# Optimization experiments

Measured on AMD Instinct MI355X. Metric: run time of the kernel, lower is better.

The kernel has to match this reference:

```python
import jax, jax.numpy as jnp
import numpy as np


def _mha(x, pos, wq, bq, wk, bk, wv, bv, num_heads):
    # x: (B, S, Din); pos: (S, Din); w*: (Din, Dout); b*: (Dout,)
    x = x + pos  # learned positional embedding, broadcast over batch
    q = x @ wq + bq
    k = x @ wk + bk
    v = x @ wv + bv
    B, S, O = q.shape
    hd = O // num_heads
    q = q.reshape(B, S, num_heads, hd)
    k = k.reshape(B, S, num_heads, hd)
    v = v.reshape(B, S, num_heads, hd)
    scores = jnp.einsum('bshd,bthd->bhst', q, k) / jnp.sqrt(jnp.asarray(hd, x.dtype))
    attn = jax.nn.softmax(scores, axis=-1)
    out = jnp.einsum('bhst,bthd->bshd', attn, v)
    return out.reshape(B, S, O)


def setup_inputs() -> dict:
    key = jax.random.key(0)
    ks = jax.random.split(key, 16)
    B = 16384
    s = 0.3
    f32 = jnp.float32
    return {
        'state': jax.random.normal(ks[0], (B, 100), f32),
        # intraframe attention: Din=1, Dout=2, seq=10, heads=2
        'pos_intra': jax.random.normal(ks[1], (10, 1), f32) * s,
        'wq_intra': jax.random.normal(ks[2], (1, 2), f32) * s,
        'bq_intra': jnp.zeros((2,), f32),
        'wk_intra': jax.random.normal(ks[3], (1, 2), f32) * s,
        'bk_intra': jnp.zeros((2,), f32),
        'wv_intra': jax.random.normal(ks[4], (1, 2), f32) * s,
        'bv_intra': jnp.zeros((2,), f32),
        # interframe attention: Din=20, Dout=21, seq=10, heads=1
        'pos_inter': jax.random.normal(ks[5], (10, 20), f32) * s,
        'wq_inter': jax.random.normal(ks[6], (20, 21), f32) * s,
        'bq_inter': jnp.zeros((21,), f32),
        'wk_inter': jax.random.normal(ks[7], (20, 21), f32) * s,
        'bk_inter': jnp.zeros((21,), f32),
        'wv_inter': jax.random.normal(ks[8], (20, 21), f32) * s,
        'bv_inter': jnp.zeros((21,), f32),
    }


def reference(state, pos_intra, wq_intra, bq_intra, wk_intra, bk_intra,
              wv_intra, bv_intra, pos_inter, wq_inter, bq_inter, wk_inter,
              bk_inter, wv_inter, bv_inter):
    B = state.shape[0]
    # per-sample reshape (10,10,1) fused across the batch: (B*10 frames, 10 tokens, 1 feat)
    frames = state.reshape(B * 10, 10, 1)
    intra = _mha(frames, pos_intra, wq_intra, bq_intra, wk_intra, bk_intra,
                 wv_intra, bv_intra, num_heads=2)          # (B*10, 10, 2)
    x = intra.reshape(B, 10, 20)                            # (B, frames=10, 20)
    out = _mha(x, pos_inter, wq_inter, bq_inter, wk_inter, bk_inter,
               wv_inter, bv_inter, num_heads=1)             # (B, 10, 21)
    return out
```

## Files before the change

kernel.cpp:

```cpp
#include <hip/hip_runtime.h>

typedef __fp16 h2 __attribute__((ext_vector_type(2)));
typedef __fp16 h4 __attribute__((ext_vector_type(4)));
typedef __fp16 h8 __attribute__((ext_vector_type(8)));
typedef float  f4 __attribute__((ext_vector_type(4)));

#if __has_builtin(__builtin_amdgcn_fdot2)
#define FDOT2(a, b, c) __builtin_amdgcn_fdot2((a), (b), (c), false)
#else
#define FDOT2(a, b, c) ((c) + (float)(a)[0] * (float)(b)[0] + (float)(a)[1] * (float)(b)[1])
#endif

#define SPB 32
#define NT  320

struct SMa {
    __fp16 X [320 * 32];
    __fp16 WT[80 * 32];
    __fp16 pad_[640];
};
union UHead { SMa a; float sout[SPB * 210]; };

__global__ __launch_bounds__(NT, 2)
void crazy_attn_kernel(const float* __restrict__ state,
                       const float* __restrict__ pos_intra,
                       const float* __restrict__ wq_i, const float* __restrict__ bq_i,
                       const float* __restrict__ wk_i, const float* __restrict__ bk_i,
                       const float* __restrict__ wv_i, const float* __restrict__ bv_i,
                       const float* __restrict__ pos_inter,
                       const float* __restrict__ wq, const float* __restrict__ bq,
                       const float* __restrict__ wk, const float* __restrict__ bk,
                       const float* __restrict__ wv, const float* __restrict__ bv,
                       float* __restrict__ out, int B)
{
    __shared__ UHead uh;
    __shared__ __fp16 QKV[320 * 80];

    const int tid  = threadIdx.x;
    const int samp = tid / 10;
    const int r    = tid - samp * 10;
    const int gs   = blockIdx.x * SPB + samp;
    const int gsc  = (gs < B) ? gs : (B - 1);

    if (tid < 80) {
        const int c  = tid;
        const int g  = c / 24;
        const int cc = c - g * 24;
        const bool valid = (g < 3) && (cc < 21);
        const float* W  = (g == 1) ? wk : (g == 2) ? wv : wq;
        const float* Bb = (g == 1) ? bk : (g == 2) ? bv : bq;
        union { uint4 u4[4]; h2 hh[16]; } T;
        #pragma unroll
        for (int p = 0; p < 16; ++p) {
            const int j0 = 2 * p, j1 = 2 * p + 1;
            float lo = 0.f, hi = 0.f;
            if (valid) {
                lo = (j0 < 20) ? W[j0 * 21 + cc] : ((j0 == 20) ? Bb[cc] : 0.f);
                hi = (j1 < 20) ? W[j1 * 21 + cc] : ((j1 == 20) ? Bb[cc] : 0.f);
            }
            T.hh[p] = __builtin_amdgcn_cvt_pkrtz(lo, hi);
        }
        uint4* wd = (uint4*)&uh.a.WT[c * 32];
        wd[0] = T.u4[0]; wd[1] = T.u4[1]; wd[2] = T.u4[2]; wd[3] = T.u4[3];
    }

    {
        const float* sp = state + (size_t)gsc * 100 + r * 10;
        float xv[10];
        #pragma unroll
        for (int t = 0; t < 10; ++t) xv[t] = sp[t] + pos_intra[t];
        float xmx = xv[0], xmn = xv[0];
        #pragma unroll
        for (int t = 1; t < 10; ++t) { xmx = fmaxf(xmx, xv[t]); xmn = fminf(xmn, xv[t]); }

        float x[20];
        #pragma unroll
        for (int h = 0; h < 2; ++h) {
            const float wqh = wq_i[h], bqh = bq_i[h];
            const float wkh = wk_i[h];
            const float wvh = wv_i[h], bvh = bv_i[h];
            float vh[10], cs[10];
            #pragma unroll
            for (int t = 0; t < 10; ++t) {
                vh[t] = fmaf(xv[t], wvh, bvh);
                cs[t] = fmaf(xv[t], wqh, bqh) * wkh;
            }
            #pragma unroll
            for (int s = 0; s < 10; ++s) {
                const float c  = cs[s];
                const float mx = c * ((c >= 0.f) ? xmx : xmn);
                const float cL = c * 1.44269504f;
                const float mL = mx * 1.44269504f;
                float sum = 0.f, o = 0.f;
                #pragma unroll
                for (int t = 0; t < 10; ++t) {
                    const float e = __builtin_amdgcn_exp2f(fmaf(cL, xv[t], -mL));
                    sum += e; o = fmaf(e, vh[t], o);
                }
                x[s * 2 + h] = o * __builtin_amdgcn_rcpf(sum);
            }
        }
        const float* prow = pos_inter + r * 20;
        union { uint4 u4[4]; h2 hh[16]; } XR;
        #pragma unroll
        for (int p = 0; p < 10; ++p)
            XR.hh[p] = __builtin_amdgcn_cvt_pkrtz(x[2 * p] + prow[2 * p],
                                                  x[2 * p + 1] + prow[2 * p + 1]);
        XR.hh[10] = __builtin_amdgcn_cvt_pkrtz(1.0f, 0.f);
        const h2 z = __builtin_amdgcn_cvt_pkrtz(0.f, 0.f);
        XR.hh[11] = z; XR.hh[12] = z; XR.hh[13] = z; XR.hh[14] = z; XR.hh[15] = z;
        uint4* xd = (uint4*)&uh.a.X[(samp * 10 + r) * 32];
        xd[0] = XR.u4[0]; xd[1] = XR.u4[1]; xd[2] = XR.u4[2]; xd[3] = XR.u4[3];
    }
    __syncthreads();

    {
        const int l  = tid & 63;
        const int w  = tid >> 6;
        const int lr = l & 15, lh = l >> 4;
        h8 afrag[5];
        #pragma unroll
        for (int mt = 0; mt < 5; ++mt)
            afrag[mt] = *(const h8*)&uh.a.WT[(mt * 16 + lr) * 32 + lh * 8];
        #pragma unroll
        for (int i = 0; i < 4; ++i) {
            const int nt   = 4 * w + i;
            const int xrow = nt * 16 + lr;
            const h8 bfrag = *(const h8*)&uh.a.X[xrow * 32 + lh * 8];
            #pragma unroll
            for (int mt = 0; mt < 5; ++mt) {
                f4 acc = {0.f, 0.f, 0.f, 0.f};
                acc = __builtin_amdgcn_mfma_f32_16x16x32_f16(afrag[mt], bfrag, acc, 0, 0, 0);
                const int c0 = mt * 16 + lh * 4;
                union { h2 p2[2]; h4 p4; } P;
                P.p2[0] = __builtin_amdgcn_cvt_pkrtz(acc[0], acc[1]);
                P.p2[1] = __builtin_amdgcn_cvt_pkrtz(acc[2], acc[3]);
                *(h4*)&QKV[xrow * 80 + c0] = P.p4;
            }
        }
    }
    __syncthreads();

    {
        const __fp16* samprows = &QKV[samp * 10 * 80];
        union { uint4 u4[3]; h2 hh[12]; } Q;
        {
            const uint4* qsrc = (const uint4*)&samprows[r * 80];
            Q.u4[0] = qsrc[0]; Q.u4[1] = qsrc[1]; Q.u4[2] = qsrc[2];
        }
        float sc[10], m = -1e30f;
        #pragma unroll
        for (int t = 0; t < 10; ++t) {
            union { uint4 u4[3]; h2 hh[12]; } K;
            const uint4* ks = (const uint4*)&samprows[t * 80 + 24];
            K.u4[0] = ks[0]; K.u4[1] = ks[1]; K.u4[2] = ks[2];
            float d = 0.f;
            #pragma unroll
            for (int p = 0; p < 11; ++p) d = FDOT2(Q.hh[p], K.hh[p], d);
            d *= 0.21821789023599239f;
            sc[t] = d; m = fmaxf(m, d);
        }
        float sum = 0.f;
        #pragma unroll
        for (int t = 0; t < 10; ++t) {
            sc[t] = __builtin_amdgcn_exp2f((sc[t] - m) * 1.44269504f);
            sum += sc[t];
        }
        const float inv = __builtin_amdgcn_rcpf(sum);

        float acc[21];
        #pragma unroll
        for (int c = 0; c < 21; ++c) acc[c] = 0.f;
        #pragma unroll
        for (int t = 0; t < 10; ++t) {
            union { uint4 u4[3]; h2 hh[12]; } V;
            const uint4* vs = (const uint4*)&samprows[t * 80 + 48];
            V.u4[0] = vs[0]; V.u4[1] = vs[1]; V.u4[2] = vs[2];
            const float a = sc[t] * inv;
            #pragma unroll
            for (int c = 0; c < 21; ++c)
                acc[c] = fmaf(a, (float)V.hh[c >> 1][c & 1], acc[c]);
        }
        float* dst = &uh.sout[(samp * 10 + r) * 21];
        #pragma unroll
        for (int c = 0; c < 21; ++c) dst[c] = acc[c];
    }
    __syncthreads();

    {
        const int samp0 = blockIdx.x * SPB;
        const int nrem  = B - samp0;
        const int nval  = ((nrem < SPB) ? nrem : SPB) * 210;
        float* gdst = out + (size_t)samp0 * 210;
        if (nval == SPB * 210) {
            #pragma unroll
            for (int i = tid; i < SPB * 210 / 4; i += NT)
                ((f4*)gdst)[i] = ((const f4*)uh.sout)[i];
        } else {
            for (int i = tid; i < nval; i += NT) gdst[i] = uh.sout[i];
        }
    }
}

extern "C" void kernel_launch(void* const* d_in, const int* in_sizes, int n_in,
                              void* d_out, int out_size, void* d_ws, size_t ws_size,
                              hipStream_t stream) {
    const float* state     = (const float*)d_in[0];
    const float* pos_intra = (const float*)d_in[1];
    const float* wq_i      = (const float*)d_in[2];
    const float* bq_i      = (const float*)d_in[3];
    const float* wk_i      = (const float*)d_in[4];
    const float* bk_i      = (const float*)d_in[5];
    const float* wv_i      = (const float*)d_in[6];
    const float* bv_i      = (const float*)d_in[7];
    const float* pos_inter = (const float*)d_in[8];
    const float* wq        = (const float*)d_in[9];
    const float* bq        = (const float*)d_in[10];
    const float* wk        = (const float*)d_in[11];
    const float* bk        = (const float*)d_in[12];
    const float* wv        = (const float*)d_in[13];
    const float* bv        = (const float*)d_in[14];
    float* outp = (float*)d_out;

    const int B = in_sizes[0] / 100;
    const int grid = (B + SPB - 1) / SPB;
    hipLaunchKernelGGL(crazy_attn_kernel, dim3(grid), dim3(NT), 0, stream,
                       state, pos_intra, wq_i, bq_i, wk_i, bk_i, wv_i, bv_i,
                       pos_inter, wq, bq, wk, bk, wv, bv, outp, B);
}
```

Measured before the change: 27.06 us.

## Split each attention row across lane pairs with DPP reductions, doubling block threads

Doubles threads per block from 320 to 640. Each row's work in the intraframe and interframe attention is now split between two adjacent lanes: each lane handles half of the query positions or keys. Partial max, sum and output accumulators are combined with a DPP xor-1 lane swap. The MFMA stage gives each wave 2 tiles instead of 4. The intent is more parallelism and latency hiding per sample, at the cost of duplicated loads of xv/Q, extra cross-lane ops and a higher launch-bounds occupancy target that may constrain registers.

After: 25.97 us. 1.04x faster.

```diff
diff --git a/kernel.cpp b/kernel.cpp
--- a/kernel.cpp
+++ b/kernel.cpp
@@ -12,7 +12,12 @@
 #endif
 
 #define SPB 32
-#define NT  320
+#define NT  640
+
+__device__ __forceinline__ float dpp_xor1(float x) {
+    int i = __builtin_amdgcn_mov_dpp(__float_as_int(x), 0xB1, 0xF, 0xF, true);
+    return __int_as_float(i);
+}
 
 struct SMa {
     __fp16 X [320 * 32];
@@ -21,7 +26,7 @@
 };
 union UHead { SMa a; float sout[SPB * 210]; };
 
-__global__ __launch_bounds__(NT, 2)
+__global__ __launch_bounds__(NT, 5)
 void crazy_attn_kernel(const float* __restrict__ state,
                        const float* __restrict__ pos_intra,
                        const float* __restrict__ wq_i, const float* __restrict__ bq_i,
@@ -37,8 +42,9 @@
     __shared__ __fp16 QKV[320 * 80];
 
     const int tid  = threadIdx.x;
-    const int samp = tid / 10;
-    const int r    = tid - samp * 10;
+    const int e    = tid & 1;
+    const int rr   = (tid >> 1) % 10;
+    const int samp = tid / 20;
     const int gs   = blockIdx.x * SPB + samp;
     const int gsc  = (gs < B) ? gs : (B - 1);
 
@@ -65,7 +71,7 @@
     }
 
     {
-        const float* sp = state + (size_t)gsc * 100 + r * 10;
+        const float* sp = state + (size_t)gsc * 100 + rr * 10;
         float xv[10];
         #pragma unroll
         for (int t = 0; t < 10; ++t) xv[t] = sp[t] + pos_intra[t];
@@ -73,44 +79,47 @@
         #pragma unroll
         for (int t = 1; t < 10; ++t) { xmx = fmaxf(xmx, xv[t]); xmn = fminf(xmn, xv[t]); }
 
-        float x[20];
+        float res[2][5];
         #pragma unroll
         for (int h = 0; h < 2; ++h) {
             const float wqh = wq_i[h], bqh = bq_i[h];
             const float wkh = wk_i[h];
             const float wvh = wv_i[h], bvh = bv_i[h];
-            float vh[10], cs[10];
-            #pragma unroll
-            for (int t = 0; t < 10; ++t) {
-                vh[t] = fmaf(xv[t], wvh, bvh);
-                cs[t] = fmaf(xv[t], wqh, bqh) * wkh;
-            }
-            #pragma unroll
-            for (int s = 0; s < 10; ++s) {
-                const float c  = cs[s];
+            float vh[10];
+            #pragma unroll
+            for (int t = 0; t < 10; ++t) vh[t] = fmaf(xv[t], wvh, bvh);
+            #pragma unroll
+            for (int si = 0; si < 5; ++si) {
+                const float c0 = fmaf(xv[2 * si],     wqh, bqh) * wkh;
+                const float c1 = fmaf(xv[2 * si + 1], wqh, bqh) * wkh;
+                const float c  = e ? c1 : c0;
                 const float mx = c * ((c >= 0.f) ? xmx : xmn);
                 const float cL = c * 1.44269504f;
                 const float mL = mx * 1.44269504f;
                 float sum = 0.f, o = 0.f;
                 #pragma unroll
                 for (int t = 0; t < 10; ++t) {
-                    const float e = __builtin_amdgcn_exp2f(fmaf(cL, xv[t], -mL));
-                    sum += e; o = fmaf(e, vh[t], o);
+                    const float ex = __builtin_amdgcn_exp2f(fmaf(cL, xv[t], -mL));
+                    sum += ex; o = fmaf(ex, vh[t], o);
                 }
-                x[s * 2 + h] = o * __builtin_amdgcn_rcpf(sum);
+                res[h][si] = o * __builtin_amdgcn_rcpf(sum);
             }
         }
-        const float* prow = pos_inter + r * 20;
-        union { uint4 u4[4]; h2 hh[16]; } XR;
-        #pragma unroll
-        for (int p = 0; p < 10; ++p)
-            XR.hh[p] = __builtin_amdgcn_cvt_pkrtz(x[2 * p] + prow[2 * p],
-                                                  x[2 * p + 1] + prow[2 * p + 1]);
-        XR.hh[10] = __builtin_amdgcn_cvt_pkrtz(1.0f, 0.f);
-        const h2 z = __builtin_amdgcn_cvt_pkrtz(0.f, 0.f);
-        XR.hh[11] = z; XR.hh[12] = z; XR.hh[13] = z; XR.hh[14] = z; XR.hh[15] = z;
-        uint4* xd = (uint4*)&uh.a.X[(samp * 10 + r) * 32];
-        xd[0] = XR.u4[0]; xd[1] = XR.u4[1]; xd[2] = XR.u4[2]; xd[3] = XR.u4[3];
+        __fp16* xrow = &uh.a.X[(samp * 10 + rr) * 32];
+        const float* prow = pos_inter + rr * 20;
+        #pragma unroll
+        for (int si = 0; si < 5; ++si) {
+            const int s = 2 * si + e;
+            *(h2*)&xrow[2 * s] = __builtin_amdgcn_cvt_pkrtz(res[0][si] + prow[2 * s],
+                                                            res[1][si] + prow[2 * s + 1]);
+        }
+        const h2 z  = __builtin_amdgcn_cvt_pkrtz(0.f, 0.f);
+        const h2 bz = __builtin_amdgcn_cvt_pkrtz(1.0f, 0.f);
+        #pragma unroll
+        for (int j = 0; j < 3; ++j) {
+            const int k = 20 + 2 * (3 * e + j);
+            *(h2*)&xrow[k] = (e == 0 && j == 0) ? bz : z;
+        }
     }
     __syncthreads();
 
@@ -123,8 +132,8 @@
         for (int mt = 0; mt < 5; ++mt)
             afrag[mt] = *(const h8*)&uh.a.WT[(mt * 16 + lr) * 32 + lh * 8];
         #pragma unroll
-        for (int i = 0; i < 4; ++i) {
-            const int nt   = 4 * w + i;
+        for (int i = 0; i < 2; ++i) {
+            const int nt   = 2 * w + i;
             const int xrow = nt * 16 + lr;
             const h8 bfrag = *(const h8*)&uh.a.X[xrow * 32 + lh * 8];
             #pragma unroll
@@ -145,45 +154,55 @@
         const __fp16* samprows = &QKV[samp * 10 * 80];
         union { uint4 u4[3]; h2 hh[12]; } Q;
         {
-            const uint4* qsrc = (const uint4*)&samprows[r * 80];
+            const uint4* qsrc = (const uint4*)&samprows[rr * 80];
             Q.u4[0] = qsrc[0]; Q.u4[1] = qsrc[1]; Q.u4[2] = qsrc[2];
         }
-        float sc[10], m = -1e30f;
-        #pragma unroll
-        for (int t = 0; t < 10; ++t) {
+        float mysc[5];
+        #pragma unroll
+        for (int i = 0; i < 5; ++i) {
+            const int t = 2 * i + e;
             union { uint4 u4[3]; h2 hh[12]; } K;
             const uint4* ks = (const uint4*)&samprows[t * 80 + 24];
             K.u4[0] = ks[0]; K.u4[1] = ks[1]; K.u4[2] = ks[2];
             float d = 0.f;
             #pragma unroll
             for (int p = 0; p < 11; ++p) d = FDOT2(Q.hh[p], K.hh[p], d);
-            d *= 0.21821789023599239f;
-            sc[t] = d; m = fmaxf(m, d);
-        }
-        float sum = 0.f;
-        #pragma unroll
-        for (int t = 0; t < 10; ++t) {
-            sc[t] = __builtin_amdgcn_exp2f((sc[t] - m) * 1.44269504f);
-            sum += sc[t];
-        }
+            mysc[i] = d * 0.21821789023599239f;
+        }
+        float mymax = mysc[0];
+        #pragma unroll
+        for (int i = 1; i < 5; ++i) mymax = fmaxf(mymax, mysc[i]);
+        const float m = fmaxf(mymax, dpp_xor1(mymax));
+        float pe[5], psum = 0.f;
+        #pragma unroll
+        for (int i = 0; i < 5; ++i) {
+            pe[i] = __builtin_amdgcn_exp2f((mysc[i] - m) * 1.44269504f);
+            psum += pe[i];
+        }
+        const float sum = psum + dpp_xor1(psum);
         const float inv = __builtin_amdgcn_rcpf(sum);
 
         float acc[21];
         #pragma unroll
         for (int c = 0; c < 21; ++c) acc[c] = 0.f;
         #pragma unroll
-        for (int t = 0; t < 10; ++t) {
+        for (int i = 0; i < 5; ++i) {
+            const int t = 2 * i + e;
             union { uint4 u4[3]; h2 hh[12]; } V;
             const uint4* vs = (const uint4*)&samprows[t * 80 + 48];
             V.u4[0] = vs[0]; V.u4[1] = vs[1]; V.u4[2] = vs[2];
-            const float a = sc[t] * inv;
+            const float a = pe[i] * inv;
             #pragma unroll
             for (int c = 0; c < 21; ++c)
                 acc[c] = fmaf(a, (float)V.hh[c >> 1][c & 1], acc[c]);
         }
-        float* dst = &uh.sout[(samp * 10 + r) * 21];
-        #pragma unroll
-        for (int c = 0; c < 21; ++c) dst[c] = acc[c];
+        #pragma unroll
+        for (int c = 0; c < 21; ++c) acc[c] += dpp_xor1(acc[c]);
+        if (e == 0) {
+            float* dst = &uh.sout[(samp * 10 + rr) * 21];
+            #pragma unroll
+            for (int c = 0; c < 21; ++c) dst[c] = acc[c];
+        }
     }
     __syncthreads();
 
@@ -193,7 +212,6 @@
         const int nval  = ((nrem < SPB) ? nrem : SPB) * 210;
         float* gdst = out + (size_t)samp0 * 210;
         if (nval == SPB * 210) {
-            #pragma unroll
             for (int i = tid; i < SPB * 210 / 4; i += NT)
                 ((f4*)gdst)[i] = ((const f4*)uh.sout)[i];
         } else {
```
